# Kernel optimization log

Measured on AMD Instinct MI355X. Metric: run time of the kernel, lower is better.

The kernel has to match this reference:

```python
import jax, jax.numpy as jnp
import numpy as np

B, N, C = 16, 1025, 1024
H, D = 16, 64          # num_heads, head_dim
NPT = 1                # num_prefix_tokens
EPS = 1e-6
SCALE = D ** -0.5


def layer_norm(x, g, b, eps=EPS):
    mu = jnp.mean(x, axis=-1, keepdims=True)
    var = jnp.mean(jnp.square(x - mu), axis=-1, keepdims=True)
    return (x - mu) * jax.lax.rsqrt(var + eps) * g + b


def rot(x):
    # interleaved rotate-half: out[..., ::2] = -x[..., 1::2]; out[..., 1::2] = x[..., ::2]
    x2 = x.reshape(*x.shape[:-1], -1, 2)
    return jnp.stack([-x2[..., 1], x2[..., 0]], axis=-1).reshape(x.shape)


def apply_rot_embed_cat(x, emb):
    # emb: (N_spatial, 2*D) = [sin | cos]
    sin_emb, cos_emb = jnp.split(emb, 2, axis=-1)
    return x * cos_emb + rot(x) * sin_emb


def setup_inputs() -> dict:
    key = jax.random.key(0)
    ks = jax.random.split(key, 12)
    s = 0.02
    return {
        "x": jax.random.normal(ks[0], (B, N, C), jnp.float32),
        "rope": jax.random.normal(ks[1], (N - NPT, 2 * D), jnp.float32),
        "qkv_w": jax.random.normal(ks[2], (3 * C, C), jnp.float32) * s,
        "q_bias": jax.random.normal(ks[3], (C,), jnp.float32) * s,
        "k_bias": jnp.zeros((C,), jnp.float32),  # registered buffer, always zero
        "v_bias": jax.random.normal(ks[4], (C,), jnp.float32) * s,
        "qn_g": jnp.ones((D,), jnp.float32),
        "qn_b": jnp.zeros((D,), jnp.float32),
        "kn_g": jnp.ones((D,), jnp.float32),
        "kn_b": jnp.zeros((D,), jnp.float32),
        "norm_g": jnp.ones((C,), jnp.float32),
        "norm_b": jnp.zeros((C,), jnp.float32),
        "proj_w": jax.random.normal(ks[5], (C, C), jnp.float32) * s,
        "proj_b": jnp.zeros((C,), jnp.float32),
    }


def reference(x, rope, qkv_w, q_bias, k_bias, v_bias, qn_g, qn_b, kn_g, kn_b,
              norm_g, norm_b, proj_w, proj_b):
    b, n, c = x.shape
    qkv_bias = jnp.concatenate([q_bias, k_bias, v_bias])
    qkv = jnp.einsum('bnc,oc->bno', x, qkv_w) + qkv_bias          # (B,N,3C)
    qkv = qkv.reshape(b, n, 3, H, D).transpose(2, 0, 3, 1, 4)     # (3,B,H,N,D)
    q, k, v = qkv[0], qkv[1], qkv[2]
    # per-head QK layernorm over head_dim
    q = layer_norm(q, qn_g, qn_b)
    k = layer_norm(k, kn_g, kn_b)
    # RoPE on spatial tokens only (prefix tokens excluded)
    q = jnp.concatenate([q[:, :, :NPT], apply_rot_embed_cat(q[:, :, NPT:], rope)], axis=2)
    k = jnp.concatenate([k[:, :, :NPT], apply_rot_embed_cat(k[:, :, NPT:], rope)], axis=2)
    # scaled dot product attention
    attn = jnp.einsum('bhqd,bhkd->bhqk', q * SCALE, k)
    attn = jax.nn.softmax(attn, axis=-1)
    out = jnp.einsum('bhqk,bhkd->bhqd', attn, v)                  # (B,H,N,D)
    out = out.transpose(0, 2, 1, 3).reshape(b, n, c)              # (B,N,C)
    out = layer_norm(out, norm_g, norm_b)                         # scale_norm
    out = jnp.einsum('bnc,oc->bno', out, proj_w) + proj_b
    return out
```

## Files before the change

### kernel.cpp

```cpp
#include <hip/hip_runtime.h>
#include <hip/hip_bf16.h>

#define B_ 16
#define N_ 1025
#define C_ 1024
#define H_ 16
#define D_ 64
#define M_ (B_ * N_)
#define EPS_ 1e-6f
#define SCALE_ 0.125f
#define VTS_ 1088

typedef __attribute__((ext_vector_type(8))) short bf16x8;
typedef __attribute__((ext_vector_type(4))) float f32x4;
typedef __attribute__((ext_vector_type(2))) unsigned int u32x2;
typedef unsigned short u16;
typedef unsigned int u32;

__device__ inline float bf2f(u16 h) {
    union { u32 u; float f; } c; c.u = ((u32)h) << 16; return c.f;
}
__device__ inline u16 f2bf(float f) {
    union { u32 u; float f; } c; c.f = f;
    u32 r = c.u + 0x7FFF + ((c.u >> 16) & 1);
    return (u16)(r >> 16);
}
__device__ inline u32 cvtpk(float lo, float hi) {
    u32 r;
    asm("v_cvt_pk_bf16_f32 %0, %1, %2" : "=v"(r) : "v"(lo), "v"(hi));
    return r;
}

__device__ inline void gload16(const void* g, void* l) {
    __builtin_amdgcn_global_load_lds(
        (const __attribute__((address_space(1))) void*)g,
        (__attribute__((address_space(3))) void*)l, 16, 0, 0);
}

__global__ __launch_bounds__(256) void k_convert(
    const void* __restrict__ src, u16* __restrict__ dst, long n,
    const u32* __restrict__ gbits)
{
    const int f = (gbits[0] == 0x3F800000u) ? 1 : 0;
    long i0 = ((long)blockIdx.x * 256 + threadIdx.x) * 4;
    long stride = (long)gridDim.x * 1024;
    if (f) {
        const float* s = (const float*)src;
        for (long i = i0; i < n; i += stride) {
#pragma unroll
            for (int j = 0; j < 4; ++j) dst[i + j] = f2bf(s[i + j]);
        }
    } else {
        const u16* s = (const u16*)src;
        for (long i = i0; i < n; i += stride) {
#pragma unroll
            for (int j = 0; j < 4; ++j) dst[i + j] = s[i + j];
        }
    }
}

__global__ __launch_bounds__(256) void k_convert_small(
    const void* s0, const void* s1, const void* s2, const void* s3,
    const void* s4, const void* s5, const void* s6, const void* s7,
    const void* s8, const void* s9, u16* __restrict__ dst,
    const u32* __restrict__ gbits)
{
    const int f = (gbits[0] == 0x3F800000u) ? 1 : 0;
    int i = blockIdx.x * 256 + threadIdx.x;
    if (i >= 6400) return;
    const void* src; int off;
    if      (i < 1024) { src = s0; off = i; }
    else if (i < 2048) { src = s1; off = i - 1024; }
    else if (i < 3072) { src = s2; off = i - 2048; }
    else if (i < 3136) { src = s3; off = i - 3072; }
    else if (i < 3200) { src = s4; off = i - 3136; }
    else if (i < 3264) { src = s5; off = i - 3200; }
    else if (i < 3328) { src = s6; off = i - 3264; }
    else if (i < 4352) { src = s7; off = i - 3328; }
    else if (i < 5376) { src = s8; off = i - 4352; }
    else               { src = s9; off = i - 5376; }
    dst[i] = f ? f2bf(((const float*)src)[off]) : ((const u16*)src)[off];
}

__global__ __launch_bounds__(256) void k_qkv(
    const u16* __restrict__ x, const u16* __restrict__ wmat,
    const u16* __restrict__ qbias, const u16* __restrict__ kbias,
    const u16* __restrict__ vbias,
    u16* __restrict__ q, u16* __restrict__ kk, u16* __restrict__ vv)
{
    __shared__ __attribute__((aligned(16))) u16 As[128 * 32];
    __shared__ __attribute__((aligned(16))) u16 Bs[128 * 32];
    const int t  = threadIdx.x;
    const int bid = blockIdx.x;
    const int wg = (bid & 7) * 387 + (bid >> 3);
    const int m0 = (wg / 24) * 128;
    const int n0 = (wg % 24) * 128;
    const int w  = t >> 6;
    const int ln = t & 15;
    const int qd = (t & 63) >> 4;
    const int wr = (w >> 1) * 64;
    const int wc = (w & 1) * 64;

    f32x4 acc[4][4] = {};

    const int srow = t >> 2;
    const int scol = (t & 3) * 8;
    int ar0 = m0 + srow;       if (ar0 >= M_) ar0 = M_ - 1;
    int ar1 = m0 + 64 + srow;  if (ar1 >= M_) ar1 = M_ - 1;
    const u16* ap0 = x + (size_t)ar0 * C_ + scol;
    const u16* ap1 = x + (size_t)ar1 * C_ + scol;
    const u16* bp0 = wmat + (size_t)(n0 + srow) * C_ + scol;
    const u16* bp1 = wmat + (size_t)(n0 + 64 + srow) * C_ + scol;
    u16* lA0 = &As[t * 8];
    u16* lA1 = &As[2048 + t * 8];
    u16* lB0 = &Bs[t * 8];
    u16* lB1 = &Bs[2048 + t * 8];

    for (int k0 = 0; k0 < C_; k0 += 32) {
        gload16(ap0 + k0, lA0);
        gload16(ap1 + k0, lA1);
        gload16(bp0 + k0, lB0);
        gload16(bp1 + k0, lB1);
        __syncthreads();
        bf16x8 a[4], b[4];
#pragma unroll
        for (int i = 0; i < 4; ++i)
            a[i] = *(const bf16x8*)&As[(wr + i * 16 + ln) * 32 + qd * 8];
#pragma unroll
        for (int j = 0; j < 4; ++j)
            b[j] = *(const bf16x8*)&Bs[(wc + j * 16 + ln) * 32 + qd * 8];
#pragma unroll
        for (int i = 0; i < 4; ++i)
#pragma unroll
            for (int j = 0; j < 4; ++j)
                acc[i][j] = __builtin_amdgcn_mfma_f32_16x16x32_bf16(a[i], b[j], acc[i][j], 0, 0, 0);
        __syncthreads();
    }

    u16* Ts = (w == 3) ? Bs : &As[w * 1152];
    const int obase = n0 + wc;
    const int part = obase >> 10;
    const int c0 = obase & 1023;
    const int hh = c0 >> 6;
    const u16* bias = (part == 0) ? qbias : (part == 1) ? kbias : vbias;
    u16* dst = (part == 0) ? q : (part == 1) ? kk : vv;
    const int lrow = (t & 63) >> 2;
    const int lchk = t & 3;
#pragma unroll
    for (int i = 0; i < 4; ++i) {
#pragma unroll
        for (int j = 0; j < 4; ++j) {
            float bv = bf2f(bias[c0 + j * 16 + ln]);
#pragma unroll
            for (int r = 0; r < 4; ++r)
                Ts[(qd * 4 + r) * 72 + j * 16 + ln] = f2bf(acc[i][j][r] + bv);
        }
        int m = m0 + wr + i * 16 + lrow;
        if (m < M_) {
            int bb = m / N_;
            int n = m - bb * N_;
            bf16x8 x0 = *(const bf16x8*)&Ts[lrow * 72 + lchk * 16];
            bf16x8 x1 = *(const bf16x8*)&Ts[lrow * 72 + lchk * 16 + 8];
            u16* dp = dst + (((size_t)(bb * H_ + hh)) * N_ + n) * D_ + lchk * 16;
            *(bf16x8*)dp = x0;
            *(bf16x8*)(dp + 8) = x1;
        }
    }
}

__global__ __launch_bounds__(256) void k_lnvt(
    u16* __restrict__ qbuf, u16* __restrict__ kbuf,
    const u16* __restrict__ qg, const u16* __restrict__ qb,
    const u16* __restrict__ kg, const u16* __restrict__ kbt,
    const u16* __restrict__ rope,
    const u16* __restrict__ v, u16* __restrict__ vt)
{
    __shared__ __attribute__((aligned(16))) u16 T[64 * 72];
    const int blk = blockIdx.x;
    const int t = threadIdx.x;

    if (blk >= 131200) {
        const int vb = blk - 131200;
        const int kb = vb % 17;
        const int bh = vb / 17;
        const int k0 = kb * 64;
        const size_t src = (size_t)bh * N_ * D_;
        const size_t dstb = (size_t)bh * D_ * VTS_;
#pragma unroll
        for (int c = 0; c < 2; ++c) {
            int id = c * 256 + t;
            int gk = id >> 3;
            int d0 = (id & 7) * 8;
            int gka = k0 + gk; if (gka > N_ - 1) gka = N_ - 1;
            bf16x8 x = *(const bf16x8*)(v + src + (size_t)gka * D_ + d0);
            int col = d0 ^ (8 * ((gk & 7) ^ (gk >> 3)));
            *(bf16x8*)&T[gk * 72 + col] = x;
        }
        __syncthreads();
#pragma unroll
        for (int c = 0; c < 2; ++c) {
            int id = c * 256 + t;
            int d   = id >> 3;
            int kk0 = (id & 7) * 8;
            bf16x8 pk;
#pragma unroll
            for (int j = 0; j < 8; ++j) {
                int key = kk0 + j;
                int col = d ^ (8 * ((key & 7) ^ (key >> 3)));
                pk[j] = (short)T[key * 72 + col];
            }
            *(bf16x8*)(vt + dstb + (size_t)d * VTS_ + k0 + kk0) = pk;
        }
        return;
    }

    const int isq = (blk < 65600);
    const int rblk = isq ? blk : blk - 65600;
    u16* buf = isq ? qbuf : kbuf;
    const u16* g = isq ? qg : kg;
    const u16* bt = isq ? qb : kbt;
    const float scale = isq ? SCALE_ : 1.0f;

    int wid = rblk * 4 + (t >> 6);
    int d = t & 63;
    if (wid >= B_ * H_ * N_) return;
    int n = wid % N_;
    u16* row = buf + (size_t)wid * 64;

    float xv = bf2f(row[d]);
    float s = xv;
#pragma unroll
    for (int off = 32; off; off >>= 1) s += __shfl_xor(s, off);
    float mu = s * (1.f / 64.f);
    float dv = xv - mu;
    float s2 = dv * dv;
#pragma unroll
    for (int off = 32; off; off >>= 1) s2 += __shfl_xor(s2, off);
    float var = s2 * (1.f / 64.f);
    float y = dv * rsqrtf(var + EPS_) * bf2f(g[d]) + bf2f(bt[d]);

    if (n >= 1) {
        const u16* rp = rope + (size_t)(n - 1) * 128;
        float sn = bf2f(rp[d]);
        float cs = bf2f(rp[64 + d]);
        float part = __shfl_xor(y, 1);
        float rot = (d & 1) ? part : -part;
        y = y * cs + rot * sn;
    }
    row[d] = f2bf(y * scale);
}

__global__ __launch_bounds__(576) void k_attn(
    const u16* __restrict__ q, const u16* __restrict__ k,
    const u16* __restrict__ vt, u16* __restrict__ out)
{
    __shared__ __attribute__((aligned(16))) u16 Ks[64 * 72];
    __shared__ __attribute__((aligned(16))) u16 Vs[64 * 72];
    __shared__ __attribute__((aligned(16))) u16 Pt[9][16 * 72];

    const int t  = threadIdx.x;
    const int w  = t >> 6;
    const int l  = t & 63;
    const int ln = t & 15;
    const int qd = l >> 4;

    const int p  = blockIdx.x;
    const int g  = (p & 7) + 8 * ((p >> 3) >> 2);
    const int qt = (p >> 3) & 3;
    const int b = g >> 4, h = g & 15;
    const size_t kbase = (size_t)g * N_ * D_;
    const size_t vbase = (size_t)g * D_ * VTS_;
    const int qw = qt * 288 + w * 32;

    bf16x8 qa[2][2];
#pragma unroll
    for (int a = 0; a < 2; ++a) {
        int row = qw + a * 16 + ln; if (row > N_ - 1) row = N_ - 1;
        const u16* qp = q + kbase + (size_t)row * D_;
        qa[a][0] = *(const bf16x8*)(qp + qd * 8);
        qa[a][1] = *(const bf16x8*)(qp + 32 + qd * 8);
    }

    f32x4 o_acc[2][4] = {};
    float m_run[2] = { -1e30f, -1e30f };
    float l_run[2] = { 0.f, 0.f };
    const f32x4 zf = { 0.f, 0.f, 0.f, 0.f };

    const int skey = t >> 3;
    const int sdg  = t & 7;

    bf16x8 pk = {}, pv = {};
    if (w < 8) {
        pk = *(const bf16x8*)(k + kbase + (size_t)skey * D_ + sdg * 8);
        pv = *(const bf16x8*)(vt + vbase + (size_t)skey * VTS_ + sdg * 8);
    }

    for (int k0 = 0; k0 < N_; k0 += 64) {
        if (w < 8) {
            *(bf16x8*)&Ks[skey * 72 + sdg * 8] = pk;
            *(bf16x8*)&Vs[skey * 72 + sdg * 8] = pv;
        }
        __syncthreads();

        const int k1 = k0 + 64;
        if (w < 8 && k1 < N_) {
            int gk = k1 + skey; if (gk > N_ - 1) gk = N_ - 1;
            pk = *(const bf16x8*)(k + kbase + (size_t)gk * D_ + sdg * 8);
            pv = *(const bf16x8*)(vt + vbase + (size_t)skey * VTS_ + k1 + sdg * 8);
        }

        bf16x8 kf[4][2];
#pragma unroll
        for (int ks = 0; ks < 4; ++ks) {
            kf[ks][0] = *(const bf16x8*)&Ks[(ks * 16 + ln) * 72 + qd * 8];
            kf[ks][1] = *(const bf16x8*)&Ks[(ks * 16 + ln) * 72 + 32 + qd * 8];
        }

        f32x4 s2[2][4];
        __builtin_amdgcn_s_setprio(1);
#pragma unroll
        for (int a = 0; a < 2; ++a)
#pragma unroll
            for (int ks = 0; ks < 4; ++ks) {
                s2[a][ks] = __builtin_amdgcn_mfma_f32_16x16x32_bf16(kf[ks][0], qa[a][0], zf, 0, 0, 0);
                s2[a][ks] = __builtin_amdgcn_mfma_f32_16x16x32_bf16(kf[ks][1], qa[a][1], s2[a][ks], 0, 0, 0);
            }
        __builtin_amdgcn_s_setprio(0);

        if (k0 + 64 > N_) {
#pragma unroll
            for (int a = 0; a < 2; ++a)
#pragma unroll
                for (int ks = 0; ks < 4; ++ks)
#pragma unroll
                    for (int r = 0; r < 4; ++r)
                        if (k0 + 16 * ks + 4 * qd + r > N_ - 1) s2[a][ks][r] = -1e30f;
        }

        float mx[2];
#pragma unroll
        for (int a = 0; a < 2; ++a) {
            float t0 = fmaxf(fmaxf(s2[a][0][0], s2[a][0][1]), fmaxf(s2[a][0][2], s2[a][0][3]));
            float t1 = fmaxf(fmaxf(s2[a][1][0], s2[a][1][1]), fmaxf(s2[a][1][2], s2[a][1][3]));
            float t2 = fmaxf(fmaxf(s2[a][2][0], s2[a][2][1]), fmaxf(s2[a][2][2], s2[a][2][3]));
            float t3 = fmaxf(fmaxf(s2[a][3][0], s2[a][3][1]), fmaxf(s2[a][3][2], s2[a][3][3]));
            float m = fmaxf(fmaxf(t0, t1), fmaxf(t2, t3));
            m = fmaxf(m, __shfl_xor(m, 16));
            m = fmaxf(m, __shfl_xor(m, 32));
            mx[a] = m;
        }

        bf16x8 pf[2][2];
#pragma unroll
        for (int a = 0; a < 2; ++a) {
            if (__any(mx[a] > m_run[a])) {
                float mn = fmaxf(m_run[a], mx[a]);
                float al = __expf(m_run[a] - mn);
                m_run[a] = mn;
                l_run[a] *= al;
#pragma unroll
                for (int nt = 0; nt < 4; ++nt)
#pragma unroll
                    for (int r = 0; r < 4; ++r)
                        o_acc[a][nt][r] *= al;
            }
            const float mcur = m_run[a];
            float rs = 0.f;
#pragma unroll
            for (int ks = 0; ks < 4; ++ks)
#pragma unroll
                for (int r = 0; r < 4; ++r) {
                    s2[a][ks][r] = __expf(s2[a][ks][r] - mcur);
                    rs += s2[a][ks][r];
                }
            rs += __shfl_xor(rs, 16);
            rs += __shfl_xor(rs, 32);
            l_run[a] += rs;

            u16* pt = &Pt[w][0];
#pragma unroll
            for (int ks = 0; ks < 4; ++ks) {
                u32x2 pr;
                pr.x = cvtpk(s2[a][ks][0], s2[a][ks][1]);
                pr.y = cvtpk(s2[a][ks][2], s2[a][ks][3]);
                *(u32x2*)&pt[ln * 72 + 16 * ks + 4 * qd] = pr;
            }
            pf[a][0] = *(const bf16x8*)&pt[ln * 72 + qd * 8];
            pf[a][1] = *(const bf16x8*)&pt[ln * 72 + 32 + qd * 8];
        }

        __builtin_amdgcn_s_setprio(1);
#pragma unroll
        for (int nt = 0; nt < 4; ++nt) {
            bf16x8 v0 = *(const bf16x8*)&Vs[(nt * 16 + ln) * 72 + qd * 8];
            bf16x8 v1 = *(const bf16x8*)&Vs[(nt * 16 + ln) * 72 + 32 + qd * 8];
#pragma unroll
            for (int a = 0; a < 2; ++a) {
                o_acc[a][nt] = __builtin_amdgcn_mfma_f32_16x16x32_bf16(v0, pf[a][0], o_acc[a][nt], 0, 0, 0);
                o_acc[a][nt] = __builtin_amdgcn_mfma_f32_16x16x32_bf16(v1, pf[a][1], o_acc[a][nt], 0, 0, 0);
            }
        }
        __builtin_amdgcn_s_setprio(0);
        __syncthreads();
    }

#pragma unroll
    for (int a = 0; a < 2; ++a) {
        float lr = l_run[a];
        u16* pt = &Pt[w][0];
#pragma unroll
        for (int nt = 0; nt < 4; ++nt) {
            u32x2 pr;
            pr.x = cvtpk(o_acc[a][nt][0] / lr, o_acc[a][nt][1] / lr);
            pr.y = cvtpk(o_acc[a][nt][2] / lr, o_acc[a][nt][3] / lr);
            *(u32x2*)&pt[ln * 72 + nt * 16 + qd * 4] = pr;
        }
        int row = l >> 2, chunk = l & 3;
        int n = qw + a * 16 + row;
        if (n < N_) {
            bf16x8 x0 = *(const bf16x8*)&pt[row * 72 + chunk * 16];
            bf16x8 x1 = *(const bf16x8*)&pt[row * 72 + chunk * 16 + 8];
            u16* op = out + ((size_t)b * N_ + n) * C_ + h * 64 + chunk * 16;
            *(bf16x8*)op = x0;
            *(bf16x8*)(op + 8) = x1;
        }
    }
}

__global__ __launch_bounds__(256) void k_ln(
    const u16* __restrict__ in, const u16* __restrict__ g,
    const u16* __restrict__ bt, u16* __restrict__ outb)
{
    __shared__ float red[8];
    const int row = blockIdx.x;
    const int t = threadIdx.x;
    const u16* p = in + (size_t)row * C_;

    float vals[4];
    float s = 0.f;
#pragma unroll
    for (int i = 0; i < 4; ++i) { vals[i] = bf2f(p[t + i * 256]); s += vals[i]; }
#pragma unroll
    for (int off = 32; off; off >>= 1) s += __shfl_xor(s, off);
    if ((t & 63) == 0) red[t >> 6] = s;
    __syncthreads();
    float mu = (red[0] + red[1] + red[2] + red[3]) * (1.f / 1024.f);
    float s2 = 0.f;
#pragma unroll
    for (int i = 0; i < 4; ++i) { float d = vals[i] - mu; s2 += d * d; }
#pragma unroll
    for (int off = 32; off; off >>= 1) s2 += __shfl_xor(s2, off);
    __syncthreads();
    if ((t & 63) == 0) red[t >> 6] = s2;
    __syncthreads();
    float var = (red[0] + red[1] + red[2] + red[3]) * (1.f / 1024.f);
    float rs = rsqrtf(var + EPS_);
#pragma unroll
    for (int i = 0; i < 4; ++i) {
        int cidx = t + i * 256;
        float y = (vals[i] - mu) * rs * bf2f(g[cidx]) + bf2f(bt[cidx]);
        outb[(size_t)row * C_ + cidx] = f2bf(y);
    }
}

__global__ __launch_bounds__(256) void k_proj(
    const u16* __restrict__ y, const u16* __restrict__ wmat,
    const u16* __restrict__ bias, void* __restrict__ out,
    const u32* __restrict__ gbits)
{
    __shared__ __attribute__((aligned(16))) u16 As[128 * 32];
    __shared__ __attribute__((aligned(16))) u16 Bs[128 * 32];
    const int t  = threadIdx.x;
    const int bid = blockIdx.x;
    const int wg = (bid & 7) * 129 + (bid >> 3);
    const int m0 = (wg >> 3) * 128;
    const int n0 = (wg & 7) * 128;
    const int w  = t >> 6;
    const int ln = t & 15;
    const int qd = (t & 63) >> 4;
    const int wr = (w >> 1) * 64;
    const int wc = (w & 1) * 64;

    f32x4 acc[4][4] = {};

    const int srow = t >> 2;
    const int scol = (t & 3) * 8;
    int ar0 = m0 + srow;       if (ar0 >= M_) ar0 = M_ - 1;
    int ar1 = m0 + 64 + srow;  if (ar1 >= M_) ar1 = M_ - 1;
    const u16* ap0 = y + (size_t)ar0 * C_ + scol;
    const u16* ap1 = y + (size_t)ar1 * C_ + scol;
    const u16* bp0 = wmat + (size_t)(n0 + srow) * C_ + scol;
    const u16* bp1 = wmat + (size_t)(n0 + 64 + srow) * C_ + scol;
    u16* lA0 = &As[t * 8];
    u16* lA1 = &As[2048 + t * 8];
    u16* lB0 = &Bs[t * 8];
    u16* lB1 = &Bs[2048 + t * 8];

    for (int k0 = 0; k0 < C_; k0 += 32) {
        gload16(ap0 + k0, lA0);
        gload16(ap1 + k0, lA1);
        gload16(bp0 + k0, lB0);
        gload16(bp1 + k0, lB1);
        __syncthreads();
        bf16x8 a[4], b[4];
#pragma unroll
        for (int i = 0; i < 4; ++i)
            a[i] = *(const bf16x8*)&As[(wr + i * 16 + ln) * 32 + qd * 8];
#pragma unroll
        for (int j = 0; j < 4; ++j)
            b[j] = *(const bf16x8*)&Bs[(wc + j * 16 + ln) * 32 + qd * 8];
#pragma unroll
        for (int i = 0; i < 4; ++i)
#pragma unroll
            for (int j = 0; j < 4; ++j)
                acc[i][j] = __builtin_amdgcn_mfma_f32_16x16x32_bf16(a[i], b[j], acc[i][j], 0, 0, 0);
        __syncthreads();
    }

    const int f32out = (gbits[0] == 0x3F800000u) ? 1 : 0;
#pragma unroll
    for (int j = 0; j < 4; ++j) {
        int o = n0 + wc + j * 16 + ln;
        float bv = bf2f(bias[o]);
#pragma unroll
        for (int i = 0; i < 4; ++i) {
#pragma unroll
            for (int r = 0; r < 4; ++r) {
                int m = m0 + wr + i * 16 + qd * 4 + r;
                if (m >= M_) continue;
                float val = acc[i][j][r] + bv;
                if (f32out) ((float*)out)[(size_t)m * C_ + o] = val;
                else        ((u16*)out)[(size_t)m * C_ + o] = f2bf(val);
            }
        }
    }
}

extern "C" void kernel_launch(void* const* d_in, const int* in_sizes, int n_in,
                              void* d_out, int out_size, void* d_ws, size_t ws_size,
                              hipStream_t stream)
{
    char* ws = (char*)d_ws;
    u16* arena = (u16*)(ws + 256);

    const long X_OFF = 0,            X_N = (long)M_ * C_;
    const long R_OFF = X_OFF + X_N,  R_N = (long)(N_ - 1) * 2 * D_;
    const long W_OFF = R_OFF + R_N,  W_N = (long)3 * C_ * C_;
    const long P_OFF = W_OFF + W_N,  P_N = (long)C_ * C_;
    const long S_OFF = P_OFF + P_N;
    const long ARENA_N = S_OFF + 6400;

    u16* xb   = arena + X_OFF;
    u16* ropb = arena + R_OFF;
    u16* qkvw = arena + W_OFF;
    u16* pw   = arena + P_OFF;
    u16* qb   = arena + S_OFF;
    u16* kb   = qb + 1024;
    u16* vb   = kb + 1024;
    u16* qng  = vb + 1024;
    u16* qnb  = qng + 64;
    u16* kng  = qnb + 64;
    u16* knb  = kng + 64;
    u16* ng   = knb + 64;
    u16* nb   = ng + 1024;
    u16* pb   = nb + 1024;

    char* after = (char*)(arena + ARENA_N);
    const size_t sz = (size_t)B_ * H_ * N_ * D_ * 2;
    u16* qbuf = (u16*)after;
    u16* kbuf = (u16*)(after + sz);
    u16* vbuf = (u16*)(after + 2 * sz);
    u16* vtb  = (u16*)(after + 3 * sz);
    u16* ao   = xb;
    u16* ybuf = qbuf;

    const u32* gbits = (const u32*)d_in[10];

    k_convert<<<4096, 256, 0, stream>>>(d_in[0], xb, X_N, gbits);
    k_convert<<<128, 256, 0, stream>>>(d_in[1], ropb, R_N, gbits);
    k_convert<<<2048, 256, 0, stream>>>(d_in[2], qkvw, W_N, gbits);
    k_convert<<<1024, 256, 0, stream>>>(d_in[12], pw, P_N, gbits);
    k_convert_small<<<25, 256, 0, stream>>>(
        d_in[3], d_in[4], d_in[5], d_in[6], d_in[7], d_in[8], d_in[9],
        d_in[10], d_in[11], d_in[13], qb, gbits);

    k_qkv<<<3096, 256, 0, stream>>>(xb, qkvw, qb, kb, vb, qbuf, kbuf, vbuf);

    k_lnvt<<<135552, 256, 0, stream>>>(qbuf, kbuf, qng, qnb, kng, knb, ropb,
                                       vbuf, vtb);

    k_attn<<<B_ * H_ * 4, 576, 0, stream>>>(qbuf, kbuf, vtb, ao);

    k_ln<<<M_, 256, 0, stream>>>(ao, ng, nb, ybuf);

    k_proj<<<1032, 256, 0, stream>>>(ybuf, pw, pb, d_out, gbits);
}
```

Measured before the change: 623.9 us.

## Merge conversion kernels into one launch and vectorize QK layernorm/RoPE per 8-lane row

Folds the five separate input-conversion launches into a single kernel that walks a concatenated index space over all inputs, writing into the contiguous arena. Rewrites the Q/K layernorm+RoPE path so each row is handled by 8 lanes with 16-byte vector loads and stores instead of one lane per element, using shuffle butterflies plus in-register reductions. This cuts launch count and the block count for the layernorm stage by a large factor, reducing scalar memory traffic and launch overhead, at the cost of more registers per thread and branchy index mapping in the merged converter.

```diff
diff --git a/kernel.cpp b/kernel.cpp
--- a/kernel.cpp
+++ b/kernel.cpp
@@ -37,49 +37,56 @@
         (__attribute__((address_space(3))) void*)l, 16, 0, 0);
 }
 
-__global__ __launch_bounds__(256) void k_convert(
-    const void* __restrict__ src, u16* __restrict__ dst, long n,
-    const u32* __restrict__ gbits)
+__global__ __launch_bounds__(256) void k_convert_all(
+    const void* sA, const void* sB, const void* sC, const void* sD,
+    const void* t0, const void* t1, const void* t2, const void* t3,
+    const void* t4, const void* t5, const void* t6, const void* t7,
+    const void* t8, const void* t9,
+    u16* __restrict__ dst, const u32* __restrict__ gbits)
 {
     const int f = (gbits[0] == 0x3F800000u) ? 1 : 0;
+    const long NX = (long)M_ * C_;
+    const long NR = (long)(N_ - 1) * 2 * D_;
+    const long NW = (long)3 * C_ * C_;
+    const long NP = (long)C_ * C_;
+    const long E0 = NX, E1 = E0 + NR, E2 = E1 + NW, E3 = E2 + NP, E4 = E3 + 6400;
     long i0 = ((long)blockIdx.x * 256 + threadIdx.x) * 4;
     long stride = (long)gridDim.x * 1024;
-    if (f) {
-        const float* s = (const float*)src;
-        for (long i = i0; i < n; i += stride) {
-#pragma unroll
-            for (int j = 0; j < 4; ++j) dst[i + j] = f2bf(s[i + j]);
-        }
-    } else {
-        const u16* s = (const u16*)src;
-        for (long i = i0; i < n; i += stride) {
-#pragma unroll
-            for (int j = 0; j < 4; ++j) dst[i + j] = s[i + j];
-        }
-    }
-}
-
-__global__ __launch_bounds__(256) void k_convert_small(
-    const void* s0, const void* s1, const void* s2, const void* s3,
-    const void* s4, const void* s5, const void* s6, const void* s7,
-    const void* s8, const void* s9, u16* __restrict__ dst,
-    const u32* __restrict__ gbits)
-{
-    const int f = (gbits[0] == 0x3F800000u) ? 1 : 0;
-    int i = blockIdx.x * 256 + threadIdx.x;
-    if (i >= 6400) return;
-    const void* src; int off;
-    if      (i < 1024) { src = s0; off = i; }
-    else if (i < 2048) { src = s1; off = i - 1024; }
-    else if (i < 3072) { src = s2; off = i - 2048; }
-    else if (i < 3136) { src = s3; off = i - 3072; }
-    else if (i < 3200) { src = s4; off = i - 3136; }
-    else if (i < 3264) { src = s5; off = i - 3200; }
-    else if (i < 3328) { src = s6; off = i - 3264; }
-    else if (i < 4352) { src = s7; off = i - 3328; }
-    else if (i < 5376) { src = s8; off = i - 4352; }
-    else               { src = s9; off = i - 5376; }
-    dst[i] = f ? f2bf(((const float*)src)[off]) : ((const u16*)src)[off];
+    for (long i = i0; i < E4; i += stride) {
+        const void* src; long off;
+        if      (i < E0) { src = sA; off = i; }
+        else if (i < E1) { src = sB; off = i - E0; }
+        else if (i < E2) { src = sC; off = i - E1; }
+        else if (i < E3) { src = sD; off = i - E2; }
+        else {
+#pragma unroll
+            for (int j = 0; j < 4; ++j) {
+                long e = i + j - E3;
+                const void* ss; long o2;
+                if      (e < 1024) { ss = t0; o2 = e; }
+                else if (e < 2048) { ss = t1; o2 = e - 1024; }
+                else if (e < 3072) { ss = t2; o2 = e - 2048; }
+                else if (e < 3136) { ss = t3; o2 = e - 3072; }
+                else if (e < 3200) { ss = t4; o2 = e - 3136; }
+                else if (e < 3264) { ss = t5; o2 = e - 3200; }
+                else if (e < 3328) { ss = t6; o2 = e - 3264; }
+                else if (e < 4352) { ss = t7; o2 = e - 3328; }
+                else if (e < 5376) { ss = t8; o2 = e - 4352; }
+                else               { ss = t9; o2 = e - 5376; }
+                dst[i + j] = f ? f2bf(((const float*)ss)[o2]) : ((const u16*)ss)[o2];
+            }
+            continue;
+        }
+        if (f) {
+            const float* s = (const float*)src;
+#pragma unroll
+            for (int j = 0; j < 4; ++j) dst[i + j] = f2bf(s[off + j]);
+        } else {
+            const u16* s = (const u16*)src;
+#pragma unroll
+            for (int j = 0; j < 4; ++j) dst[i + j] = s[off + j];
+        }
+    }
 }
 
 __global__ __launch_bounds__(256) void k_qkv(
@@ -179,8 +186,8 @@
     const int blk = blockIdx.x;
     const int t = threadIdx.x;
 
-    if (blk >= 131200) {
-        const int vb = blk - 131200;
+    if (blk >= 16400) {
+        const int vb = blk - 16400;
         const int kb = vb % 17;
         const int bh = vb / 17;
         const int k0 = kb * 64;
@@ -214,40 +221,93 @@
         return;
     }
 
-    const int isq = (blk < 65600);
-    const int rblk = isq ? blk : blk - 65600;
+    const int isq = (blk < 8200);
+    const int rblk = isq ? blk : blk - 8200;
     u16* buf = isq ? qbuf : kbuf;
-    const u16* g = isq ? qg : kg;
-    const u16* bt = isq ? qb : kbt;
+    const u16* gg = isq ? qg : kg;
+    const u16* bb = isq ? qb : kbt;
     const float scale = isq ? SCALE_ : 1.0f;
 
-    int wid = rblk * 4 + (t >> 6);
-    int d = t & 63;
-    if (wid >= B_ * H_ * N_) return;
-    int n = wid % N_;
+    const int l  = t & 63;
+    const int w  = t >> 6;
+    const int sl = l & 7;
+    const int wid = rblk * 32 + w * 8 + (l >> 3);
+    const int n = wid % N_;
     u16* row = buf + (size_t)wid * 64;
 
-    float xv = bf2f(row[d]);
-    float s = xv;
-#pragma unroll
-    for (int off = 32; off; off >>= 1) s += __shfl_xor(s, off);
-    float mu = s * (1.f / 64.f);
-    float dv = xv - mu;
-    float s2 = dv * dv;
-#pragma unroll
-    for (int off = 32; off; off >>= 1) s2 += __shfl_xor(s2, off);
-    float var = s2 * (1.f / 64.f);
-    float y = dv * rsqrtf(var + EPS_) * bf2f(g[d]) + bf2f(bt[d]);
+    bf16x8 xr = *(const bf16x8*)(row + sl * 8);
+    float xv[8], s[8];
+#pragma unroll
+    for (int j = 0; j < 8; ++j) { xv[j] = bf2f((u16)xr[j]); s[j] = xv[j]; }
+
+#pragma unroll
+    for (int j = 0; j < 8; ++j) s[j] += __shfl_xor(s[j], 4);
+#pragma unroll
+    for (int j = 0; j < 8; ++j) s[j] += __shfl_xor(s[j], 2);
+#pragma unroll
+    for (int j = 0; j < 8; ++j) s[j] += __shfl_xor(s[j], 1);
+    {
+        float tt[8];
+#pragma unroll
+        for (int j = 0; j < 8; ++j) tt[j] = s[j] + s[j ^ 4];
+#pragma unroll
+        for (int j = 0; j < 8; ++j) s[j] = tt[j] + tt[j ^ 2];
+#pragma unroll
+        for (int j = 0; j < 8; ++j) tt[j] = s[j] + s[j ^ 1];
+#pragma unroll
+        for (int j = 0; j < 8; ++j) s[j] = tt[j];
+    }
+    float mu = s[0] * (1.f / 64.f);
+
+    float dv[8], s2[8];
+#pragma unroll
+    for (int j = 0; j < 8; ++j) { dv[j] = xv[j] - mu; s2[j] = dv[j] * dv[j]; }
+#pragma unroll
+    for (int j = 0; j < 8; ++j) s2[j] += __shfl_xor(s2[j], 4);
+#pragma unroll
+    for (int j = 0; j < 8; ++j) s2[j] += __shfl_xor(s2[j], 2);
+#pragma unroll
+    for (int j = 0; j < 8; ++j) s2[j] += __shfl_xor(s2[j], 1);
+    {
+        float tt[8];
+#pragma unroll
+        for (int j = 0; j < 8; ++j) tt[j] = s2[j] + s2[j ^ 4];
+#pragma unroll
+        for (int j = 0; j < 8; ++j) s2[j] = tt[j] + tt[j ^ 2];
+#pragma unroll
+        for (int j = 0; j < 8; ++j) tt[j] = s2[j] + s2[j ^ 1];
+#pragma unroll
+        for (int j = 0; j < 8; ++j) s2[j] = tt[j];
+    }
+    float var = s2[0] * (1.f / 64.f);
+    float rinv = rsqrtf(var + EPS_);
+
+    bf16x8 gr = *(const bf16x8*)(gg + sl * 8);
+    bf16x8 br = *(const bf16x8*)(bb + sl * 8);
+    float y[8];
+#pragma unroll
+    for (int j = 0; j < 8; ++j)
+        y[j] = dv[j] * rinv * bf2f((u16)gr[j]) + bf2f((u16)br[j]);
 
     if (n >= 1) {
         const u16* rp = rope + (size_t)(n - 1) * 128;
-        float sn = bf2f(rp[d]);
-        float cs = bf2f(rp[64 + d]);
-        float part = __shfl_xor(y, 1);
-        float rot = (d & 1) ? part : -part;
-        y = y * cs + rot * sn;
-    }
-    row[d] = f2bf(y * scale);
+        bf16x8 snr = *(const bf16x8*)(rp + sl * 8);
+        bf16x8 csr = *(const bf16x8*)(rp + 64 + sl * 8);
+        float y2[8];
+#pragma unroll
+        for (int j = 0; j < 8; ++j) {
+            float part = y[j ^ 1];
+            float rot = (j & 1) ? part : -part;
+            y2[j] = y[j] * bf2f((u16)csr[j]) + rot * bf2f((u16)snr[j]);
+        }
+#pragma unroll
+        for (int j = 0; j < 8; ++j) y[j] = y2[j];
+    }
+
+    bf16x8 outv;
+#pragma unroll
+    for (int j = 0; j < 8; ++j) outv[j] = (short)f2bf(y[j] * scale);
+    *(bf16x8*)(row + sl * 8) = outv;
 }
 
 __global__ __launch_bounds__(576) void k_attn(
@@ -576,18 +636,16 @@
 
     const u32* gbits = (const u32*)d_in[10];
 
-    k_convert<<<4096, 256, 0, stream>>>(d_in[0], xb, X_N, gbits);
-    k_convert<<<128, 256, 0, stream>>>(d_in[1], ropb, R_N, gbits);
-    k_convert<<<2048, 256, 0, stream>>>(d_in[2], qkvw, W_N, gbits);
-    k_convert<<<1024, 256, 0, stream>>>(d_in[12], pw, P_N, gbits);
-    k_convert_small<<<25, 256, 0, stream>>>(
+    k_convert_all<<<8192, 256, 0, stream>>>(
+        d_in[0], d_in[1], d_in[2], d_in[12],
         d_in[3], d_in[4], d_in[5], d_in[6], d_in[7], d_in[8], d_in[9],
-        d_in[10], d_in[11], d_in[13], qb, gbits);
+        d_in[10], d_in[11], d_in[13],
+        arena, gbits);
 
     k_qkv<<<3096, 256, 0, stream>>>(xb, qkvw, qb, kb, vb, qbuf, kbuf, vbuf);
 
-    k_lnvt<<<135552, 256, 0, stream>>>(qbuf, kbuf, qng, qnb, kng, knb, ropb,
-                                       vbuf, vtb);
+    k_lnvt<<<20752, 256, 0, stream>>>(qbuf, kbuf, qng, qnb, kng, knb, ropb,
+                                      vbuf, vtb);
 
     k_attn<<<B_ * H_ * 4, 576, 0, stream>>>(qbuf, kbuf, vtb, ao);
 
```

After: 565.2 us. 9.4% less time.
